# Kernel tuning notes

Hardware: AMD Instinct MI355X
Metric: run time of the kernel (lower is better)

## Reference

```python
import jax, jax.numpy as jnp
import numpy as np
from jax import lax

DIM = 1024
B, N = 4, 4096


def setup_inputs() -> dict:
    key = jax.random.key(0)
    k1, k2 = jax.random.split(key)
    x = jax.random.normal(k1, (B, N, DIM), dtype=jnp.float32)
    # Linear(dim, 3*dim, bias=False): weight stored as [3*dim, dim] (torch convention)
    w_qkva = jax.random.normal(k2, (3 * DIM, DIM), dtype=jnp.float32) * (DIM ** -0.5)
    gamma = jnp.ones((DIM,), dtype=jnp.float32)  # RMSNorm gain
    return {"x": x, "w_qkva": w_qkva, "gamma": gamma}


def _rmsnorm(x, gamma):
    # lucidrains RMSNorm: F.normalize(x, dim=-1) * sqrt(dim) * gamma
    scale = jnp.asarray(x.shape[-1], x.dtype) ** 0.5
    norm = jnp.sqrt(jnp.sum(x * x, axis=-1, keepdims=True))
    return x / jnp.maximum(norm, 1e-12) * scale * gamma


def reference(x, w_qkva, gamma):
    h = _rmsnorm(x, gamma)                                  # [b, n, d]
    qkva = jnp.einsum('bnd,ed->bne', h, w_qkva)             # [b, n, 3d]
    q, kv, a = jnp.split(qkva, 3, axis=-1)                  # each [b, n, d]
    a = jax.nn.sigmoid(a)

    def binary_operator(e_i, e_j):
        a_i, kv_i = e_i
        a_j, kv_j = e_j
        return (a_j * a_i, a_j * kv_i + kv_j)

    # gated linear recurrence over the sequence axis (elementwise per channel)
    _, y = lax.associative_scan(binary_operator, (a, kv), axis=1)
    return q * y                                            # [b, n, d]
```

## Files before the change

kernel.cpp:

```cpp
#include <hip/hip_runtime.h>
#include <hip/hip_bf16.h>

#define SEQ_N 4096
#define BATCH 4
#define DIM 1024
#define M_ROWS (BATCH * SEQ_N)
#define NCOLS (3 * DIM)
#define KDIM DIM
#define CHUNK_L 16
#define NCHUNK (SEQ_N / CHUNK_L)
#define NCHANNEL (BATCH * DIM)
#define GT 32

using short8 = __attribute__((ext_vector_type(8))) short;
using f32x4  = __attribute__((ext_vector_type(4))) float;

static __device__ __forceinline__ unsigned short f2bf(float f) {
    union { float f; unsigned u; } v; v.f = f;
    unsigned r = v.u + 0x7fffu + ((v.u >> 16) & 1u);
    return (unsigned short)(r >> 16);
}
static __device__ __forceinline__ float bf2f(unsigned short s) {
    union { unsigned u; float f; } v; v.u = ((unsigned)s) << 16;
    return v.f;
}
static __device__ __forceinline__ float sigm(float x) {
    return 1.f / (1.f + __expf(-x));
}

#define WCONV_BLOCKS 3072
__global__ __launch_bounds__(256) void pre_kernel(const float* __restrict__ w,
                                                  unsigned short* __restrict__ wb,
                                                  const float* __restrict__ x,
                                                  const float* __restrict__ gamma,
                                                  unsigned short* __restrict__ h) {
    const int bid = blockIdx.x;
    const int tid = threadIdx.x;
    if (bid < WCONV_BLOCKS) {
        const int i = bid * 256 + tid;
        float4 v = reinterpret_cast<const float4*>(w)[i];
        ushort4 o;
        o.x = f2bf(v.x); o.y = f2bf(v.y); o.z = f2bf(v.z); o.w = f2bf(v.w);
        reinterpret_cast<ushort4*>(wb)[i] = o;
        return;
    }
    const int row = bid - WCONV_BLOCKS;
    const float4 v = reinterpret_cast<const float4*>(x + (size_t)row * DIM)[tid];
    float ss = v.x * v.x + v.y * v.y + v.z * v.z + v.w * v.w;
#pragma unroll
    for (int off = 32; off >= 1; off >>= 1) ss += __shfl_xor(ss, off, 64);
    __shared__ float red[4];
    if ((tid & 63) == 0) red[tid >> 6] = ss;
    __syncthreads();
    const float tot = red[0] + red[1] + red[2] + red[3];
    const float scale = 32.0f / fmaxf(sqrtf(tot), 1e-12f);
    const float4 g = reinterpret_cast<const float4*>(gamma)[tid];
    ushort4 o;
    o.x = f2bf(v.x * scale * g.x);
    o.y = f2bf(v.y * scale * g.y);
    o.z = f2bf(v.z * scale * g.z);
    o.w = f2bf(v.w * scale * g.w);
    reinterpret_cast<ushort4*>(h + (size_t)row * DIM)[tid] = o;
}

__global__ __launch_bounds__(512, 2) void gemm256_kernel(const unsigned short* __restrict__ A,
                                                         const unsigned short* __restrict__ B,
                                                         unsigned short* __restrict__ C) {
    __shared__ __align__(16) unsigned short sA[4][256][32];
    __shared__ __align__(16) unsigned short sB[4][256][32];

    const int tid  = threadIdx.x;
    const int lane = tid & 63;
    const int wave = tid >> 6;

    const int orig = blockIdx.x;
    const int swz  = (orig & 7) * 96 + (orig >> 3);
    const int ntile = swz >> 6;
    const int mtile = swz & 63;
    const int row0 = mtile * 256;
    const int col0 = ntile * 256;

    const int wm = (wave >> 2) * 128;
    const int wn = (wave & 3) * 64;
    const int fr = lane & 15;
    const int kq = lane >> 4;
    const int kqx = kq ^ ((fr >> 1) & 3);

    const int srow = tid >> 2;
    const int scol = ((tid & 3) ^ ((srow >> 1) & 3)) * 8;
    const unsigned short* aSrc = A + (size_t)(row0 + srow) * KDIM + scol;
    const unsigned short* bSrc = B + (size_t)(col0 + srow) * KDIM + scol;
    unsigned short* sAf = &sA[0][0][0];
    unsigned short* sBf = &sB[0][0][0];
    const int sdst = tid * 8;

#define STAGE_A(bs, kt, u)                                                              \
    __builtin_amdgcn_global_load_lds(                                                   \
        (const __attribute__((address_space(1))) void*)(aSrc + (size_t)(u) * 128 * KDIM + (kt) * 32), \
        (__attribute__((address_space(3))) void*)(sAf + (bs) * 8192 + (u) * 4096 + sdst), 16, 0, 0);
#define STAGE_B(bs, kt, u)                                                              \
    __builtin_amdgcn_global_load_lds(                                                   \
        (const __attribute__((address_space(1))) void*)(bSrc + (size_t)(u) * 128 * KDIM + (kt) * 32), \
        (__attribute__((address_space(3))) void*)(sBf + (bs) * 8192 + (u) * 4096 + sdst), 16, 0, 0);

    f32x4 acc[8][4] = {};

    STAGE_A(0, 0, 0); STAGE_A(0, 0, 1); STAGE_B(0, 0, 0); STAGE_B(0, 0, 1);
    STAGE_A(1, 1, 0); STAGE_A(1, 1, 1); STAGE_B(1, 1, 0); STAGE_B(1, 1, 1);
    asm volatile("s_waitcnt vmcnt(4)" ::: "memory");
    __builtin_amdgcn_sched_barrier(0);
    __builtin_amdgcn_s_barrier();

    for (int t = 0; t < GT; ++t) {
        const int b  = t & 3;
        const int bs = (t + 2) & 3;
        const bool st = (t + 2 < GT);
        const unsigned short* sAb = sAf + b * 8192;
        const unsigned short* sBb = sBf + b * 8192;

        short8 bfr[4], afr[4];
#pragma unroll
        for (int j = 0; j < 4; ++j)
            bfr[j] = *reinterpret_cast<const short8*>(sBb + (wn + j * 16 + fr) * 32 + kqx * 8);
#pragma unroll
        for (int i = 0; i < 4; ++i)
            afr[i] = *reinterpret_cast<const short8*>(sAb + (wm + i * 16 + fr) * 32 + kqx * 8);
        if (st) { STAGE_A(bs, t + 2, 0); STAGE_A(bs, t + 2, 1); }
        __builtin_amdgcn_s_barrier();
        __builtin_amdgcn_s_setprio(1);
#pragma unroll
        for (int i = 0; i < 4; ++i)
#pragma unroll
            for (int j = 0; j < 4; ++j)
                acc[i][j] = __builtin_amdgcn_mfma_f32_16x16x32_bf16(afr[i], bfr[j], acc[i][j], 0, 0, 0);
        __builtin_amdgcn_s_setprio(0);
        __builtin_amdgcn_s_barrier();

        short8 afr2[4];
#pragma unroll
        for (int i = 0; i < 4; ++i)
            afr2[i] = *reinterpret_cast<const short8*>(sAb + (wm + 64 + i * 16 + fr) * 32 + kqx * 8);
        if (st) { STAGE_B(bs, t + 2, 0); STAGE_B(bs, t + 2, 1); }
        __builtin_amdgcn_s_barrier();
        __builtin_amdgcn_s_setprio(1);
#pragma unroll
        for (int i = 0; i < 4; ++i)
#pragma unroll
            for (int j = 0; j < 4; ++j)
                acc[4 + i][j] = __builtin_amdgcn_mfma_f32_16x16x32_bf16(afr2[i], bfr[j], acc[4 + i][j], 0, 0, 0);
        __builtin_amdgcn_s_setprio(0);
        if (t < GT - 2) {
            asm volatile("s_waitcnt vmcnt(4)" ::: "memory");
        } else if (t == GT - 2) {
            asm volatile("s_waitcnt vmcnt(0)" ::: "memory");
        }
        __builtin_amdgcn_sched_barrier(0);
        __builtin_amdgcn_s_barrier();
    }
#undef STAGE_A
#undef STAGE_B

#pragma unroll
    for (int i = 0; i < 8; ++i) {
#pragma unroll
        for (int j = 0; j < 4; ++j) {
#pragma unroll
            for (int r = 0; r < 4; ++r) {
                int row = row0 + wm + i * 16 + kq * 4 + r;
                int col = col0 + wn + j * 16 + fr;
                C[(size_t)row * NCOLS + col] = f2bf(acc[i][j][r]);
            }
        }
    }
}

__global__ __launch_bounds__(256) void chunk_agg_kernel(const unsigned short* __restrict__ qkva,
                                                        float* __restrict__ Aagg,
                                                        float* __restrict__ Yagg) {
    const int c = blockIdx.x, b = blockIdx.y;
    const int d4 = threadIdx.x * 4;
    const unsigned short* base = qkva + ((size_t)b * SEQ_N + c * CHUNK_L) * NCOLS;
    float s[4] = {0.f, 0.f, 0.f, 0.f};
    float A[4] = {1.f, 1.f, 1.f, 1.f};
#pragma unroll 4
    for (int n = 0; n < CHUNK_L; ++n) {
        const ushort4 kvu = *reinterpret_cast<const ushort4*>(base + (size_t)n * NCOLS + DIM + d4);
        const ushort4 au  = *reinterpret_cast<const ushort4*>(base + (size_t)n * NCOLS + 2 * DIM + d4);
        const float kv[4] = {bf2f(kvu.x), bf2f(kvu.y), bf2f(kvu.z), bf2f(kvu.w)};
        const float av[4] = {bf2f(au.x),  bf2f(au.y),  bf2f(au.z),  bf2f(au.w)};
#pragma unroll
        for (int j = 0; j < 4; ++j) {
            const float a = sigm(av[j]);
            s[j] = fmaf(a, s[j], kv[j]);
            A[j] *= a;
        }
    }
    const int idx = c * NCHANNEL + b * DIM + d4;
    float4 Ao, Yo;
    Ao.x = A[0]; Ao.y = A[1]; Ao.z = A[2]; Ao.w = A[3];
    Yo.x = s[0]; Yo.y = s[1]; Yo.z = s[2]; Yo.w = s[3];
    *reinterpret_cast<float4*>(&Aagg[idx]) = Ao;
    *reinterpret_cast<float4*>(&Yagg[idx]) = Yo;
}

__global__ __launch_bounds__(256) void agg_scan_kernel(const float* __restrict__ Aagg,
                                                       const float* __restrict__ Yagg,
                                                       float* __restrict__ Sin) {
    const int ch = blockIdx.x * 256 + threadIdx.x;
    float s = 0.f;
#pragma unroll 8
    for (int c = 0; c < NCHUNK; ++c) {
        const float A = Aagg[c * NCHANNEL + ch];
        const float Y = Yagg[c * NCHANNEL + ch];
        Sin[c * NCHANNEL + ch] = s;
        s = fmaf(A, s, Y);
    }
}

__global__ __launch_bounds__(256) void apply_kernel(const unsigned short* __restrict__ qkva,
                                                    const float* __restrict__ Sin,
                                                    float* __restrict__ out) {
    const int c = blockIdx.x, b = blockIdx.y;
    const int d4 = threadIdx.x * 4;
    const unsigned short* base = qkva + ((size_t)b * SEQ_N + c * CHUNK_L) * NCOLS;
    float* obase = out + ((size_t)b * SEQ_N + c * CHUNK_L) * DIM;
    const float4 s0 = *reinterpret_cast<const float4*>(&Sin[c * NCHANNEL + b * DIM + d4]);
    float s[4] = {s0.x, s0.y, s0.z, s0.w};
#pragma unroll 4
    for (int n = 0; n < CHUNK_L; ++n) {
        const ushort4 qu  = *reinterpret_cast<const ushort4*>(base + (size_t)n * NCOLS + d4);
        const ushort4 kvu = *reinterpret_cast<const ushort4*>(base + (size_t)n * NCOLS + DIM + d4);
        const ushort4 au  = *reinterpret_cast<const ushort4*>(base + (size_t)n * NCOLS + 2 * DIM + d4);
        const float kv[4] = {bf2f(kvu.x), bf2f(kvu.y), bf2f(kvu.z), bf2f(kvu.w)};
        const float av[4] = {bf2f(au.x),  bf2f(au.y),  bf2f(au.z),  bf2f(au.w)};
        const float q[4]  = {bf2f(qu.x),  bf2f(qu.y),  bf2f(qu.z),  bf2f(qu.w)};
        float4 o;
#pragma unroll
        for (int j = 0; j < 4; ++j) {
            const float a = sigm(av[j]);
            s[j] = fmaf(a, s[j], kv[j]);
        }
        o.x = q[0] * s[0]; o.y = q[1] * s[1]; o.z = q[2] * s[2]; o.w = q[3] * s[3];
        *reinterpret_cast<float4*>(&obase[(size_t)n * DIM + d4]) = o;
    }
}

extern "C" void kernel_launch(void* const* d_in, const int* in_sizes, int n_in,
                              void* d_out, int out_size, void* d_ws, size_t ws_size,
                              hipStream_t stream) {
    const float* x     = (const float*)d_in[0];
    const float* w     = (const float*)d_in[1];
    const float* gamma = (const float*)d_in[2];
    float* out = (float*)d_out;

    char* ws = (char*)d_ws;
    unsigned short* wb   = (unsigned short*)(ws);
    unsigned short* h    = (unsigned short*)(ws + 6291456);
    unsigned short* qkva = (unsigned short*)(ws + 39845888);
    float* Aagg = (float*)(ws + 6291456);
    float* Yagg = (float*)(ws + 6291456 + 4194304);
    float* Sin  = (float*)(ws + 6291456 + 8388608);

    pre_kernel<<<WCONV_BLOCKS + M_ROWS, 256, 0, stream>>>(w, wb, x, gamma, h);
    gemm256_kernel<<<(M_ROWS / 256) * (NCOLS / 256), 512, 0, stream>>>(h, wb, qkva);
    chunk_agg_kernel<<<dim3(NCHUNK, BATCH), 256, 0, stream>>>(qkva, Aagg, Yagg);
    agg_scan_kernel<<<NCHANNEL / 256, 256, 0, stream>>>(Aagg, Yagg, Sin);
    apply_kernel<<<dim3(NCHUNK, BATCH), 256, 0, stream>>>(qkva, Sin, out);
}
```

Measured before the change: 294.3 us.

## Remap GEMM tile order, merge GEMM k-step phases, segment chunk-aggregate scan

```diff
diff --git a/kernel.cpp b/kernel.cpp
--- a/kernel.cpp
+++ b/kernel.cpp
@@ -74,9 +74,10 @@
     const int wave = tid >> 6;
 
     const int orig = blockIdx.x;
-    const int swz  = (orig & 7) * 96 + (orig >> 3);
-    const int ntile = swz >> 6;
-    const int mtile = swz & 63;
+    const int xcd  = orig & 7;
+    const int q    = orig >> 3;
+    const int mtile = xcd * 8 + q / 12;
+    const int ntile = q % 12;
     const int row0 = mtile * 256;
     const int col0 = ntile * 256;
 
@@ -118,37 +119,33 @@
         const unsigned short* sAb = sAf + b * 8192;
         const unsigned short* sBb = sBf + b * 8192;
 
-        short8 bfr[4], afr[4];
+        short8 bfr[4], afr[4], afr2[4];
 #pragma unroll
         for (int j = 0; j < 4; ++j)
             bfr[j] = *reinterpret_cast<const short8*>(sBb + (wn + j * 16 + fr) * 32 + kqx * 8);
 #pragma unroll
         for (int i = 0; i < 4; ++i)
             afr[i] = *reinterpret_cast<const short8*>(sAb + (wm + i * 16 + fr) * 32 + kqx * 8);
-        if (st) { STAGE_A(bs, t + 2, 0); STAGE_A(bs, t + 2, 1); }
-        __builtin_amdgcn_s_barrier();
+#pragma unroll
+        for (int i = 0; i < 4; ++i)
+            afr2[i] = *reinterpret_cast<const short8*>(sAb + (wm + 64 + i * 16 + fr) * 32 + kqx * 8);
+
+        if (st) { STAGE_A(bs, t + 2, 0); STAGE_A(bs, t + 2, 1);
+                  STAGE_B(bs, t + 2, 0); STAGE_B(bs, t + 2, 1); }
+
         __builtin_amdgcn_s_setprio(1);
 #pragma unroll
         for (int i = 0; i < 4; ++i)
 #pragma unroll
             for (int j = 0; j < 4; ++j)
                 acc[i][j] = __builtin_amdgcn_mfma_f32_16x16x32_bf16(afr[i], bfr[j], acc[i][j], 0, 0, 0);
-        __builtin_amdgcn_s_setprio(0);
-        __builtin_amdgcn_s_barrier();
-
-        short8 afr2[4];
-#pragma unroll
-        for (int i = 0; i < 4; ++i)
-            afr2[i] = *reinterpret_cast<const short8*>(sAb + (wm + 64 + i * 16 + fr) * 32 + kqx * 8);
-        if (st) { STAGE_B(bs, t + 2, 0); STAGE_B(bs, t + 2, 1); }
-        __builtin_amdgcn_s_barrier();
-        __builtin_amdgcn_s_setprio(1);
 #pragma unroll
         for (int i = 0; i < 4; ++i)
 #pragma unroll
             for (int j = 0; j < 4; ++j)
                 acc[4 + i][j] = __builtin_amdgcn_mfma_f32_16x16x32_bf16(afr2[i], bfr[j], acc[4 + i][j], 0, 0, 0);
         __builtin_amdgcn_s_setprio(0);
+
         if (t < GT - 2) {
             asm volatile("s_waitcnt vmcnt(4)" ::: "memory");
         } else if (t == GT - 2) {
@@ -206,14 +203,38 @@
 __global__ __launch_bounds__(256) void agg_scan_kernel(const float* __restrict__ Aagg,
                                                        const float* __restrict__ Yagg,
                                                        float* __restrict__ Sin) {
-    const int ch = blockIdx.x * 256 + threadIdx.x;
+    __shared__ float sA[NCHUNK][64];
+    __shared__ float sY[NCHUNK][64];
+    __shared__ float segA[4][64], segY[4][64];
+    const int t = threadIdx.x;
+    const int ch0 = blockIdx.x * 64;
+    const int j = t & 63;
+    const int g = t >> 6;
+#pragma unroll 8
+    for (int i = 0; i < 64; ++i) {
+        const int c = i * 4 + g;
+        sA[c][j] = Aagg[(size_t)c * NCHANNEL + ch0 + j];
+        sY[c][j] = Yagg[(size_t)c * NCHANNEL + ch0 + j];
+    }
+    __syncthreads();
+    float a = 1.f, y = 0.f;
+#pragma unroll 8
+    for (int i = 0; i < 64; ++i) {
+        const int c = g * 64 + i;
+        y = fmaf(sA[c][j], y, sY[c][j]);
+        a *= sA[c][j];
+    }
+    segA[g][j] = a; segY[g][j] = y;
+    __syncthreads();
     float s = 0.f;
+#pragma unroll
+    for (int gg = 0; gg < 3; ++gg)
+        if (gg < g) s = fmaf(segA[gg][j], s, segY[gg][j]);
 #pragma unroll 8
-    for (int c = 0; c < NCHUNK; ++c) {
-        const float A = Aagg[c * NCHANNEL + ch];
-        const float Y = Yagg[c * NCHANNEL + ch];
-        Sin[c * NCHANNEL + ch] = s;
-        s = fmaf(A, s, Y);
+    for (int i = 0; i < 64; ++i) {
+        const int c = g * 64 + i;
+        Sin[(size_t)c * NCHANNEL + ch0 + j] = s;
+        s = fmaf(sA[c][j], s, sY[c][j]);
     }
 }
 
@@ -224,7 +245,7 @@
     const int d4 = threadIdx.x * 4;
     const unsigned short* base = qkva + ((size_t)b * SEQ_N + c * CHUNK_L) * NCOLS;
     float* obase = out + ((size_t)b * SEQ_N + c * CHUNK_L) * DIM;
-    const float4 s0 = *reinterpret_cast<const float4*>(&Sin[c * NCHANNEL + b * DIM + d4]);
+    const float4 s0 = *reinterpret_cast<const float4*>(&Sin[(size_t)c * NCHANNEL + b * DIM + d4]);
     float s[4] = {s0.x, s0.y, s0.z, s0.w};
 #pragma unroll 4
     for (int n = 0; n < CHUNK_L; ++n) {
@@ -264,6 +285,6 @@
     pre_kernel<<<WCONV_BLOCKS + M_ROWS, 256, 0, stream>>>(w, wb, x, gamma, h);
     gemm256_kernel<<<(M_ROWS / 256) * (NCOLS / 256), 512, 0, stream>>>(h, wb, qkva);
     chunk_agg_kernel<<<dim3(NCHUNK, BATCH), 256, 0, stream>>>(qkva, Aagg, Yagg);
-    agg_scan_kernel<<<NCHANNEL / 256, 256, 0, stream>>>(Aagg, Yagg, Sin);
+    agg_scan_kernel<<<NCHANNEL / 64, 256, 0, stream>>>(Aagg, Yagg, Sin);
     apply_kernel<<<dim3(NCHUNK, BATCH), 256, 0, stream>>>(qkva, Sin, out);
 }
```

Result: faster. 273.8 us (-7.0%).
